# Performance work log

Measured on AMD Instinct MI355X. Metric: run time of the kernel, lower is better.

## Reference

```python
import jax, jax.numpy as jnp
import numpy as np

NUM_NEURONS = 8192
INPUT_SIZE = 512
OUTPUT_SIZE = 512
TAU = 10.0
G = 1.5


def setup_inputs() -> dict:
    key = jax.random.key(0)
    k1, k2, k3, k4, k5 = jax.random.split(key, 5)
    inputs = jax.random.normal(k1, (INPUT_SIZE,), dtype=jnp.float32)
    potentials = jax.random.normal(k2, (1, NUM_NEURONS), dtype=jnp.float32)
    # parameters, matching the torch init scales
    W_in = jax.random.normal(k3, (INPUT_SIZE, NUM_NEURONS), dtype=jnp.float32) * 0.1
    synapses = jax.random.normal(k4, (NUM_NEURONS, NUM_NEURONS), dtype=jnp.float32) / np.sqrt(NUM_NEURONS).astype(np.float32)
    W_out = jax.random.normal(k5, (NUM_NEURONS, OUTPUT_SIZE), dtype=jnp.float32) / np.float32(NUM_NEURONS)
    return {"inputs": inputs, "potentials": potentials, "W_in": W_in,
            "synapses": synapses, "W_out": W_out}


def reference(inputs, potentials, W_in, synapses, W_out):
    # input_map: bias-free linear, then unsqueeze to [1, N]
    drive = (inputs @ W_in)[None, :]                      # [1, N]
    # Neurons: continuous-time leaky integrator (FORCE-style)
    rates = jnp.tanh(potentials)                          # [1, N]
    pot_new = potentials + (-potentials + G * (rates @ synapses) + drive) / TAU
    gen_net = jnp.tanh(pot_new)                           # [1, N]
    # read_out: bias-free linear
    output = gen_net @ W_out                              # [1, output_size]
    return (output, pot_new)
```

## Files before the change

kernel.cpp:

```cpp
#include <hip/hip_runtime.h>
#include <math.h>

#define N_NEU   8192
#define IN_SZ   512
#define OUT_SZ  512
#define N4      (N_NEU / 4)
#define KPB     64
constexpr float TAU_INV = 0.1f;
constexpr float G_GAIN  = 1.5f;

__global__ __launch_bounds__(256)
void accum_kernel(const float* __restrict__ pot,
                  const float* __restrict__ inputs,
                  const float* __restrict__ synapses,
                  const float* __restrict__ W_in,
                  float* __restrict__ acc_buf) {
    __shared__ float xs[KPB];
    const int by = blockIdx.y;
    const float4* M;
    int k0;
    if (by < N_NEU / KPB) {
        k0 = by * KPB;
        M  = (const float4*)synapses;
        if (threadIdx.x < KPB)
            xs[threadIdx.x] = G_GAIN * tanhf(pot[k0 + threadIdx.x]);
    } else {
        k0 = (by - N_NEU / KPB) * KPB;
        M  = (const float4*)W_in;
        if (threadIdx.x < KPB)
            xs[threadIdx.x] = inputs[k0 + threadIdx.x];
    }
    __syncthreads();

    const int col4 = blockIdx.x * blockDim.x + threadIdx.x;
    const float4* Mp = M + (size_t)k0 * N4 + col4;

    float4 acc = make_float4(0.f, 0.f, 0.f, 0.f);
#pragma unroll 8
    for (int i = 0; i < KPB; ++i) {
        float  s = xs[i];
        float4 m = Mp[(size_t)i * N4];
        acc.x = fmaf(s, m.x, acc.x);
        acc.y = fmaf(s, m.y, acc.y);
        acc.z = fmaf(s, m.z, acc.z);
        acc.w = fmaf(s, m.w, acc.w);
    }

    float* yp = acc_buf + (size_t)col4 * 4;
    atomicAdd(yp + 0, acc.x);
    atomicAdd(yp + 1, acc.y);
    atomicAdd(yp + 2, acc.z);
    atomicAdd(yp + 3, acc.w);
}

#define K2_KPB   64
#define OUT4     (OUT_SZ / 4)
__global__ __launch_bounds__(128)
void finish_kernel(const float* __restrict__ pot,
                   const float* __restrict__ acc_buf,
                   const float* __restrict__ W_out,
                   float* __restrict__ out) {
    const int b = blockIdx.x;
    if (b < N_NEU / K2_KPB) {
        __shared__ float xs[K2_KPB];
        const int k0 = b * K2_KPB;
        if (threadIdx.x < K2_KPB) {
            int k = k0 + threadIdx.x;
            float p  = pot[k];
            float pn = p + (acc_buf[k] - p) * TAU_INV;
            xs[threadIdx.x] = tanhf(pn);
        }
        __syncthreads();

        const int col4 = threadIdx.x;
        const float4* Wp = (const float4*)W_out + (size_t)k0 * OUT4 + col4;
        float4 acc = make_float4(0.f, 0.f, 0.f, 0.f);
#pragma unroll 8
        for (int i = 0; i < K2_KPB; ++i) {
            float  s = xs[i];
            float4 m = Wp[(size_t)i * OUT4];
            acc.x = fmaf(s, m.x, acc.x);
            acc.y = fmaf(s, m.y, acc.y);
            acc.z = fmaf(s, m.z, acc.z);
            acc.w = fmaf(s, m.w, acc.w);
        }
        float* op = out + (size_t)col4 * 4;
        atomicAdd(op + 0, acc.x);
        atomicAdd(op + 1, acc.y);
        atomicAdd(op + 2, acc.z);
        atomicAdd(op + 3, acc.w);
    } else {
        int j = (b - N_NEU / K2_KPB) * 128 + threadIdx.x;
        float p  = pot[j];
        float pn = p + (acc_buf[j] - p) * TAU_INV;
        out[OUT_SZ + j] = pn;
    }
}

extern "C" void kernel_launch(void* const* d_in, const int* in_sizes, int n_in,
                              void* d_out, int out_size, void* d_ws, size_t ws_size,
                              hipStream_t stream) {
    const float* inputs   = (const float*)d_in[0];
    const float* pot      = (const float*)d_in[1];
    const float* W_in     = (const float*)d_in[2];
    const float* synapses = (const float*)d_in[3];
    const float* W_out    = (const float*)d_in[4];

    float* out     = (float*)d_out;
    float* acc_buf = (float*)d_ws;

    hipMemsetAsync(acc_buf, 0, N_NEU * sizeof(float), stream);
    hipMemsetAsync(out, 0, OUT_SZ * sizeof(float), stream);

    accum_kernel<<<dim3(N4 / 256, N_NEU / KPB + IN_SZ / KPB), dim3(256), 0, stream>>>(
        pot, inputs, synapses, W_in, acc_buf);

    finish_kernel<<<dim3(N_NEU / K2_KPB + N_NEU / 128), dim3(128), 0, stream>>>(
        pot, acc_buf, W_out, out);
}
```

Before: 407.6 us.

## Replace atomic accumulation with partial-sum buffer and drop memsets

The matvec kernel now writes each block's partial sums to a workspace buffer (TILES x N floats) instead of doing atomicAdds into a zeroed accumulator. The finish kernel reduces the 136 partials per neuron itself. Zeroing of the output is folded into the first kernel, which removes both memset launches. This trades about 4.5 MB of extra partial-buffer traffic and a redundant reduction in both finish branches for the removal of atomic contention and launch overhead. K2_KPB also doubles to 128.

```diff
diff --git a/kernel.cpp b/kernel.cpp
--- a/kernel.cpp
+++ b/kernel.cpp
@@ -5,7 +5,13 @@
 #define IN_SZ   512
 #define OUT_SZ  512
 #define N4      (N_NEU / 4)
+#define OUT4    (OUT_SZ / 4)
 #define KPB     64
+#define SYN_TILES (N_NEU / KPB)
+#define WIN_TILES (IN_SZ / KPB)
+#define TILES     (SYN_TILES + WIN_TILES)
+#define K2_KPB  128
+#define OTILES  (N_NEU / K2_KPB)
 constexpr float TAU_INV = 0.1f;
 constexpr float G_GAIN  = 1.5f;
 
@@ -14,25 +20,26 @@
                   const float* __restrict__ inputs,
                   const float* __restrict__ synapses,
                   const float* __restrict__ W_in,
-                  float* __restrict__ acc_buf) {
+                  float4* __restrict__ P4,
+                  float* __restrict__ out) {
     __shared__ float xs[KPB];
-    const int by = blockIdx.y;
+    const int bx = blockIdx.x, by = blockIdx.y;
+    const int tid = threadIdx.x;
     const float4* M;
     int k0;
-    if (by < N_NEU / KPB) {
+    if (by < SYN_TILES) {
         k0 = by * KPB;
         M  = (const float4*)synapses;
-        if (threadIdx.x < KPB)
-            xs[threadIdx.x] = G_GAIN * tanhf(pot[k0 + threadIdx.x]);
+        if (tid < KPB) xs[tid] = G_GAIN * tanhf(pot[k0 + tid]);
     } else {
-        k0 = (by - N_NEU / KPB) * KPB;
+        k0 = (by - SYN_TILES) * KPB;
         M  = (const float4*)W_in;
-        if (threadIdx.x < KPB)
-            xs[threadIdx.x] = inputs[k0 + threadIdx.x];
+        if (tid < KPB) xs[tid] = inputs[k0 + tid];
     }
+    if (by == TILES - 1 && tid < 64) out[bx * 64 + tid] = 0.0f;
     __syncthreads();
 
-    const int col4 = blockIdx.x * blockDim.x + threadIdx.x;
+    const int col4 = bx * 256 + tid;
     const float4* Mp = M + (size_t)k0 * N4 + col4;
 
     float4 acc = make_float4(0.f, 0.f, 0.f, 0.f);
@@ -45,54 +52,56 @@
         acc.z = fmaf(s, m.z, acc.z);
         acc.w = fmaf(s, m.w, acc.w);
     }
-
-    float* yp = acc_buf + (size_t)col4 * 4;
-    atomicAdd(yp + 0, acc.x);
-    atomicAdd(yp + 1, acc.y);
-    atomicAdd(yp + 2, acc.z);
-    atomicAdd(yp + 3, acc.w);
+    P4[(size_t)(by * 8 + bx) * 256 + tid] = acc;
 }
 
-#define K2_KPB   64
-#define OUT4     (OUT_SZ / 4)
 __global__ __launch_bounds__(128)
 void finish_kernel(const float* __restrict__ pot,
-                   const float* __restrict__ acc_buf,
+                   const float* __restrict__ P,
                    const float* __restrict__ W_out,
                    float* __restrict__ out) {
     const int b = blockIdx.x;
-    if (b < N_NEU / K2_KPB) {
+    const int t = threadIdx.x;
+    if (b < OTILES) {
         __shared__ float xs[K2_KPB];
-        const int k0 = b * K2_KPB;
-        if (threadIdx.x < K2_KPB) {
-            int k = k0 + threadIdx.x;
-            float p  = pot[k];
-            float pn = p + (acc_buf[k] - p) * TAU_INV;
-            xs[threadIdx.x] = tanhf(pn);
-        }
+        const int k0  = b * K2_KPB;
+        const int bx  = k0 >> 10;
+        const int off = (k0 & 1023) + t;
+        float s = 0.f;
+#pragma unroll 8
+        for (int by = 0; by < TILES; ++by)
+            s += P[(size_t)(by * 8 + bx) * 1024 + off];
+        float p  = pot[k0 + t];
+        float pn = p + (s - p) * TAU_INV;
+        xs[t] = tanhf(pn);
         __syncthreads();
 
-        const int col4 = threadIdx.x;
-        const float4* Wp = (const float4*)W_out + (size_t)k0 * OUT4 + col4;
+        const float4* Wp = (const float4*)W_out + (size_t)k0 * OUT4 + t;
         float4 acc = make_float4(0.f, 0.f, 0.f, 0.f);
 #pragma unroll 8
         for (int i = 0; i < K2_KPB; ++i) {
-            float  s = xs[i];
-            float4 m = Wp[(size_t)i * OUT4];
-            acc.x = fmaf(s, m.x, acc.x);
-            acc.y = fmaf(s, m.y, acc.y);
-            acc.z = fmaf(s, m.z, acc.z);
-            acc.w = fmaf(s, m.w, acc.w);
+            float  sx = xs[i];
+            float4 m  = Wp[(size_t)i * OUT4];
+            acc.x = fmaf(sx, m.x, acc.x);
+            acc.y = fmaf(sx, m.y, acc.y);
+            acc.z = fmaf(sx, m.z, acc.z);
+            acc.w = fmaf(sx, m.w, acc.w);
         }
-        float* op = out + (size_t)col4 * 4;
+        float* op = out + (size_t)t * 4;
         atomicAdd(op + 0, acc.x);
         atomicAdd(op + 1, acc.y);
         atomicAdd(op + 2, acc.z);
         atomicAdd(op + 3, acc.w);
     } else {
-        int j = (b - N_NEU / K2_KPB) * 128 + threadIdx.x;
+        const int j   = (b - OTILES) * 128 + t;
+        const int bx  = j >> 10;
+        const int off = j & 1023;
+        float s = 0.f;
+#pragma unroll 8
+        for (int by = 0; by < TILES; ++by)
+            s += P[(size_t)(by * 8 + bx) * 1024 + off];
         float p  = pot[j];
-        float pn = p + (acc_buf[j] - p) * TAU_INV;
+        float pn = p + (s - p) * TAU_INV;
         out[OUT_SZ + j] = pn;
     }
 }
@@ -106,15 +115,12 @@
     const float* synapses = (const float*)d_in[3];
     const float* W_out    = (const float*)d_in[4];
 
-    float* out     = (float*)d_out;
-    float* acc_buf = (float*)d_ws;
+    float* out = (float*)d_out;
+    float* P   = (float*)d_ws;
 
-    hipMemsetAsync(acc_buf, 0, N_NEU * sizeof(float), stream);
-    hipMemsetAsync(out, 0, OUT_SZ * sizeof(float), stream);
+    accum_kernel<<<dim3(8, TILES), dim3(256), 0, stream>>>(
+        pot, inputs, synapses, W_in, (float4*)P, out);
 
-    accum_kernel<<<dim3(N4 / 256, N_NEU / KPB + IN_SZ / KPB), dim3(256), 0, stream>>>(
-        pot, inputs, synapses, W_in, acc_buf);
-
-    finish_kernel<<<dim3(N_NEU / K2_KPB + N_NEU / 128), dim3(128), 0, stream>>>(
-        pot, acc_buf, W_out, out);
+    finish_kernel<<<dim3(OTILES + N_NEU / 128), dim3(128), 0, stream>>>(
+        pot, P, W_out, out);
 }
```

After: 405.3 us. Within noise of the previous version (-0.6%).
